# Kernel tuning notes

Hardware: AMD Instinct MI355X
Metric: run time of the kernel (lower is better)

Reference implementation:

```python
import jax, jax.numpy as jnp
import numpy as np

B, LT, LE, D, H, M, BS = 4, 2048, 1024, 1024, 16, 4096, 128
HD = D // H            # head dim 64
NB = LT // BS          # 16 blocks
SINK_ITERS = 5
NEG = -1e9
SCALE = 1.0 / np.sqrt(HD).astype(np.float32)


def setup_inputs() -> dict:
    key = jax.random.key(0)
    ks = jax.random.split(key, 16)
    p = lambda k, shp: jax.random.normal(k, shp, jnp.float32) * 0.02
    return {
        "targets": jax.random.normal(ks[0], (B, LT, D), jnp.float32),
        "encoded": jax.random.normal(ks[1], (B, LE, D), jnp.float32),
        "ln1_s": jnp.ones((D,), jnp.float32), "ln1_b": jnp.zeros((D,), jnp.float32),
        "ln2_s": jnp.ones((D,), jnp.float32), "ln2_b": jnp.zeros((D,), jnp.float32),
        "ln3_s": jnp.ones((D,), jnp.float32), "ln3_b": jnp.zeros((D,), jnp.float32),
        "wq1": p(ks[2], (D, H, HD)), "wk1": p(ks[3], (D, H, HD)),
        "wv1": p(ks[4], (D, H, HD)), "wo1": p(ks[5], (H, HD, D)),
        "wsort": p(ks[6], (H, HD, NB)),
        "wq2": p(ks[7], (D, H, HD)), "wk2": p(ks[8], (D, H, HD)),
        "wv2": p(ks[9], (D, H, HD)), "wo2": p(ks[10], (H, HD, D)),
        "w1": p(ks[11], (D, M)), "b1": jnp.zeros((M,), jnp.float32),
        "w2": p(ks[12], (M, D)), "b2": jnp.zeros((D,), jnp.float32),
    }


def layer_norm(x, s, b, eps=1e-6):
    mu = jnp.mean(x, -1, keepdims=True)
    var = jnp.mean(jnp.square(x - mu), -1, keepdims=True)
    return (x - mu) * jax.lax.rsqrt(var + eps) * s + b


def causal_sinkhorn(logits):
    # logits: [B,H,NB,NB]. Causal block mask + iterative log-space row/col
    # normalization -> soft (doubly-stochastic-ish) block permutation matrix.
    mask = jnp.tril(jnp.ones((NB, NB), bool))
    la = jnp.where(mask, logits, NEG)
    for _ in range(SINK_ITERS):
        la = la - jax.nn.logsumexp(la, axis=-1, keepdims=True)
        la = jnp.where(mask, la, NEG)
        la = la - jax.nn.logsumexp(la, axis=-2, keepdims=True)
        la = jnp.where(mask, la, NEG)
    return jnp.exp(la)


def sinkhorn_self_attention(x, wq, wk, wv, wsort, wo):
    # x: [B,LT,D] -> blocked q/k/v: [B,NB,BS,H,HD]
    q = jnp.einsum('bld,dhk->blhk', x, wq).reshape(B, NB, BS, H, HD)
    k = jnp.einsum('bld,dhk->blhk', x, wk).reshape(B, NB, BS, H, HD)
    v = jnp.einsum('bld,dhk->blhk', x, wv).reshape(B, NB, BS, H, HD)
    # SortNet: sum-pooled block key representations -> block-to-block logits
    krep = jnp.sum(k, axis=2)                                   # [B,NB,H,HD]
    P = causal_sinkhorn(jnp.einsum('bnhk,hkm->bhnm', krep, wsort))  # [B,H,NB,NB]
    ks = jnp.einsum('bhij,bjshk->bishk', P, k)                  # sorted key blocks
    vs = jnp.einsum('bhij,bjshk->bishk', P, v)
    # each query block attends to (own block [causal]) ++ (sorted block)
    s_loc = jnp.einsum('bnqhk,bnshk->bhnqs', q, k) * SCALE      # [B,H,NB,BS,BS]
    s_srt = jnp.einsum('bnqhk,bnshk->bhnqs', q, ks) * SCALE
    cm = jnp.tril(jnp.ones((BS, BS), bool))
    s_loc = jnp.where(cm, s_loc, NEG)
    w = jax.nn.softmax(jnp.concatenate([s_loc, s_srt], axis=-1), axis=-1)
    o = (jnp.einsum('bhnqs,bnshk->bnqhk', w[..., :BS], v)
         + jnp.einsum('bhnqs,bnshk->bnqhk', w[..., BS:], vs))
    return jnp.einsum('blhk,hkd->bld', o.reshape(B, LT, H, HD), wo)


def cross_attention(x, kv, wq, wk, wv, wo):
    q = jnp.einsum('bld,dhk->blhk', x, wq)
    k = jnp.einsum('bld,dhk->blhk', kv, wk)
    v = jnp.einsum('bld,dhk->blhk', kv, wv)
    w = jax.nn.softmax(jnp.einsum('bqhk,bshk->bhqs', q, k) * SCALE, axis=-1)
    o = jnp.einsum('bhqs,bshk->bqhk', w, v)
    return jnp.einsum('blhk,hkd->bld', o, wo)


def reference(targets, encoded, ln1_s, ln1_b, ln2_s, ln2_b, ln3_s, ln3_b,
              wq1, wk1, wv1, wo1, wsort, wq2, wk2, wv2, wo2, w1, b1, w2, b2):
    x = layer_norm(targets, ln1_s, ln1_b)
    x = sinkhorn_self_attention(x, wq1, wk1, wv1, wsort, wo1) + targets
    y = layer_norm(x, ln2_s, ln2_b)
    y = cross_attention(y, encoded, wq2, wk2, wv2, wo2) + x
    z = layer_norm(y, ln3_s, ln3_b)
    z = jnp.dot(jax.nn.gelu(jnp.dot(z, w1) + b1), w2) + b2
    return y + z
```

## Files before the change

### kernel.cpp

```cpp
#include <hip/hip_runtime.h>

typedef unsigned short u16;
typedef unsigned int u32;
typedef __attribute__((ext_vector_type(8))) short short8;
typedef __attribute__((ext_vector_type(4))) short short4_t;
typedef __attribute__((ext_vector_type(4))) float float4_t;

#define B_ 4
#define LT_ 2048
#define LE_ 1024
#define D_ 1024
#define H_ 16
#define HD_ 64
#define NB_ 16
#define BS_ 128
#define M_ 4096
#define SCALE_ 0.125f

typedef __attribute__((address_space(1))) const void gas_t;
typedef __attribute__((address_space(3))) void las_t;

__device__ __forceinline__ float b2f(u16 u) {
  union { unsigned int i; float f; } v; v.i = ((unsigned int)u) << 16; return v.f;
}
__device__ __forceinline__ u16 f2b(float f) {
  union { float f; unsigned int i; } v; v.f = f;
  unsigned int x = v.i;
  return (u16)((x + 0x7fffu + ((x >> 16) & 1u)) >> 16);
}
__device__ __forceinline__ float gelu_f(float u) {
  float t = 0.7978845608028654f * (u + 0.044715f * u * u * u);
  float th = 1.f - 2.f / (__expf(2.f * t) + 1.f);
  return 0.5f * u * (1.f + th);
}
__device__ __forceinline__ void store_val(u16* p, float x) { *p = f2b(x); }
__device__ __forceinline__ void store_val(float* p, float x) { *p = x; }

__global__ __launch_bounds__(256)
void conv_k(const float* __restrict__ in, u16* __restrict__ out) {
  int i = (blockIdx.x * 256 + threadIdx.x) * 4;
  float4_t v = *(const float4_t*)(in + i);
  short4_t o;
  o[0] = (short)f2b(v[0]); o[1] = (short)f2b(v[1]);
  o[2] = (short)f2b(v[2]); o[3] = (short)f2b(v[3]);
  *(short4_t*)(out + i) = o;
}

__global__ __launch_bounds__(256)
void transpose_k(const float* __restrict__ in, u16* __restrict__ out, int R, int rstride) {
  __shared__ u16 tile[32][33];
  int bx = blockIdx.x * 32, by = blockIdx.y * 32;
  int tx = threadIdx.x & 31, ty = threadIdx.x >> 5;
  #pragma unroll
  for (int y = ty; y < 32; y += 8)
    tile[y][tx] = f2b(in[(size_t)(by + y) * rstride + bx + tx]);
  __syncthreads();
  #pragma unroll
  for (int y = ty; y < 32; y += 8)
    out[(size_t)(bx + y) * R + by + tx] = tile[tx][y];
}

#define NJOBS 10
struct TJobs {
  const float* src[NJOBS];
  u16* dst[NJOBS];
  int outR[NJOBS];
  int inS[NJOBS];
  int ntx[NJOBS];
  int ntiles[NJOBS];
};

__global__ __launch_bounds__(256)
void prep_k(TJobs J) {
  int t = blockIdx.x, j = 0;
  while (t >= J.ntiles[j]) { t -= J.ntiles[j]; ++j; }
  const float* in = J.src[j];
  u16* out = J.dst[j];
  const int R = J.outR[j], rstride = J.inS[j];
  const int bx = (t % J.ntx[j]) * 32, by = (t / J.ntx[j]) * 32;
  __shared__ u16 tile[32][33];
  int tx = threadIdx.x & 31, ty = threadIdx.x >> 5;
  #pragma unroll
  for (int y = ty; y < 32; y += 8)
    tile[y][tx] = f2b(in[(size_t)(by + y) * rstride + bx + tx]);
  __syncthreads();
  #pragma unroll
  for (int y = ty; y < 32; y += 8)
    out[(size_t)(bx + y) * R + by + tx] = tile[tx][y];
}

__global__ __launch_bounds__(256)
void ln_k(const float* __restrict__ x, const float* __restrict__ sw,
          const float* __restrict__ bw, u16* __restrict__ out) {
  int row = blockIdx.x, tid = threadIdx.x;
  const float* xr = x + (size_t)row * 1024 + tid * 4;
  float4_t raw = *(const float4_t*)xr;
  float v0 = raw[0], v1 = raw[1], v2 = raw[2], v3 = raw[3];
  float sum = v0 + v1 + v2 + v3;
  #pragma unroll
  for (int off = 32; off > 0; off >>= 1) sum += __shfl_down(sum, off, 64);
  __shared__ float sA[4], sB[4];
  int w = tid >> 6;
  if ((tid & 63) == 0) sA[w] = sum;
  __syncthreads();
  float mu = (sA[0] + sA[1] + sA[2] + sA[3]) * (1.f / 1024.f);
  float d0 = v0 - mu, d1 = v1 - mu, d2 = v2 - mu, d3 = v3 - mu;
  float s2 = d0 * d0 + d1 * d1 + d2 * d2 + d3 * d3;
  #pragma unroll
  for (int off = 32; off > 0; off >>= 1) s2 += __shfl_down(s2, off, 64);
  if ((tid & 63) == 0) sB[w] = s2;
  __syncthreads();
  float inv = rsqrtf((sB[0] + sB[1] + sB[2] + sB[3]) * (1.f / 1024.f) + 1e-6f);
  float4_t sv = *(const float4_t*)(sw + tid * 4);
  float4_t bv = *(const float4_t*)(bw + tid * 4);
  short4_t ov;
  ov[0] = (short)f2b(d0 * inv * sv[0] + bv[0]);
  ov[1] = (short)f2b(d1 * inv * sv[1] + bv[1]);
  ov[2] = (short)f2b(d2 * inv * sv[2] + bv[2]);
  ov[3] = (short)f2b(d3 * inv * sv[3] + bv[3]);
  *(short4_t*)(out + (size_t)row * 1024 + tid * 4) = ov;
}

template<int EPI, typename TC, int SPLIT>
__global__ __launch_bounds__(256)
void gemm_k(const u16* __restrict__ A, const u16* __restrict__ Bt,
            const float* __restrict__ bias, const float* __restrict__ res,
            TC* __restrict__ C, int M, int N, int K, size_t cstride) {
  __shared__ __align__(16) u16 lA[128 * 32];
  __shared__ __align__(16) u16 lB[128 * 32];
  const int gx = gridDim.x;
  int lin = blockIdx.y * gx + blockIdx.x;
  const int nwg = gx * gridDim.y;
  if (!(nwg & 7)) {
    const int chunk = nwg >> 3;
    lin = (lin & 7) * chunk + (lin >> 3);
  }
  const int bn = (lin % gx) * 128;
  const int bm = (lin / gx) * 128;
  const int tid = threadIdx.x;
  const int lane = tid & 63;
  const int wave = tid >> 6;
  const int wy = wave >> 1, wx = wave & 1;
  const int quad = lane >> 4, l16 = lane & 15;

  float4_t acc[4][4];
  float4_t zz = {0.f, 0.f, 0.f, 0.f};
  #pragma unroll
  for (int i = 0; i < 4; ++i)
    #pragma unroll
    for (int j = 0; j < 4; ++j) acc[i][j] = zz;

  const int r0 = tid >> 2, kc0 = (tid & 3) * 8;
  const u16* gA0 = A + (size_t)(bm + r0) * K + kc0;
  const u16* gA1 = A + (size_t)(bm + 64 + r0) * K + kc0;
  const u16* gB0 = Bt + (size_t)(bn + r0) * K + kc0;
  const u16* gB1 = Bt + (size_t)(bn + 64 + r0) * K + kc0;
  u16* lA0 = &lA[tid * 8];
  u16* lA1 = &lA[(tid + 256) * 8];
  u16* lB0 = &lB[tid * 8];
  u16* lB1 = &lB[(tid + 256) * 8];

  for (int k0 = 0; k0 < K; k0 += 32) {
    __syncthreads();
    __builtin_amdgcn_global_load_lds((gas_t*)(gA0 + k0), (las_t*)lA0, 16, 0, 0);
    __builtin_amdgcn_global_load_lds((gas_t*)(gA1 + k0), (las_t*)lA1, 16, 0, 0);
    __builtin_amdgcn_global_load_lds((gas_t*)(gB0 + k0), (las_t*)lB0, 16, 0, 0);
    __builtin_amdgcn_global_load_lds((gas_t*)(gB1 + k0), (las_t*)lB1, 16, 0, 0);
    __syncthreads();
    short8 af[4], bfr[4];
    #pragma unroll
    for (int i = 0; i < 4; ++i)
      af[i] = *(const short8*)&lA[(wy * 64 + i * 16 + l16) * 32 + quad * 8];
    #pragma unroll
    for (int j = 0; j < 4; ++j)
      bfr[j] = *(const short8*)&lB[(wx * 64 + j * 16 + l16) * 32 + quad * 8];
    #pragma unroll
    for (int i = 0; i < 4; ++i)
      #pragma unroll
      for (int j = 0; j < 4; ++j)
        acc[i][j] = __builtin_amdgcn_mfma_f32_16x16x32_bf16(af[i], bfr[j], acc[i][j], 0, 0, 0);
  }

  #pragma unroll
  for (int i = 0; i < 4; ++i) {
    int row = bm + wy * 64 + i * 16 + quad * 4;
    #pragma unroll
    for (int j = 0; j < 4; ++j) {
      int col = bn + wx * 64 + j * 16 + l16;
      TC* Cb = SPLIT ? (C + (size_t)(col >> 10) * cstride) : C;
      int ccol = SPLIT ? (col & 1023) : col;
      int cn = SPLIT ? 1024 : N;
      #pragma unroll
      for (int v = 0; v < 4; ++v) {
        float x = acc[i][j][v];
        size_t idx = (size_t)(row + v) * cn + ccol;
        if (EPI == 1) {
          x += res[idx];
        } else if (EPI == 2) {
          x = gelu_f(x + bias[col]);
        } else if (EPI == 3) {
          x += bias[col] + res[idx];
        }
        store_val(&Cb[idx], x);
      }
    }
  }
}

template<int EPI, typename TC, int SPLIT>
__global__ __launch_bounds__(512, 2)
void gemm256_k(const u16* __restrict__ A, const u16* __restrict__ Bt,
               const float* __restrict__ bias, const float* __restrict__ res,
               TC* __restrict__ C, int M, int N, int K, size_t cstride) {
  __shared__ __align__(16) u16 lA[4][256 * 32];
  __shared__ __align__(16) u16 lB[4][256 * 32];
  const int gx = gridDim.x;
  int lin = blockIdx.y * gx + blockIdx.x;
  const int nwg = gx * gridDim.y;
  if (!(nwg & 7)) {
    const int chunk = nwg >> 3;
    lin = (lin & 7) * chunk + (lin >> 3);
  }
  const int bn = (lin % gx) * 256;
  const int bm = (lin / gx) * 256;
  const int tid = threadIdx.x;
  const int lane = tid & 63;
  const int wave = tid >> 6;
  const int wy = wave >> 2, wx = wave & 3;
  const int quad = lane >> 4, l16 = lane & 15;
  const int slo = ((quad ^ ((l16 >> 1) & 3)) << 4);

  int lrow[2], kcs[2];
  #pragma unroll
  for (int u = 0; u < 2; ++u) {
    int p = (tid + u * 512) * 16;
    int lg = p ^ (((p >> 7) & 3) << 4);
    lrow[u] = lg >> 6;
    kcs[u] = (lg & 63) >> 1;
  }
  const u16* gA[2]; const u16* gB[2];
  #pragma unroll
  for (int u = 0; u < 2; ++u) {
    gA[u] = A + (size_t)(bm + lrow[u]) * K + kcs[u];
    gB[u] = Bt + (size_t)(bn + lrow[u]) * K + kcs[u];
  }
  const int NT = K >> 5;

  float4_t acc[8][4];
  float4_t zz = {0.f, 0.f, 0.f, 0.f};
  #pragma unroll
  for (int i = 0; i < 8; ++i)
    #pragma unroll
    for (int j = 0; j < 4; ++j) acc[i][j] = zz;

  #define STAGE256(TT, BUF)                                                      \
    {                                                                            \
      int kk_ = (TT) * 32;                                                       \
      __builtin_amdgcn_global_load_lds((gas_t*)(gA[0] + kk_),                    \
          (las_t*)((char*)&lA[BUF][0] + tid * 16), 16, 0, 0);                    \
      __builtin_amdgcn_global_load_lds((gas_t*)(gA[1] + kk_),                    \
          (las_t*)((char*)&lA[BUF][0] + (tid + 512) * 16), 16, 0, 0);            \
      __builtin_amdgcn_global_load_lds((gas_t*)(gB[0] + kk_),                    \
          (las_t*)((char*)&lB[BUF][0] + tid * 16), 16, 0, 0);                    \
      __builtin_amdgcn_global_load_lds((gas_t*)(gB[1] + kk_),                    \
          (las_t*)((char*)&lB[BUF][0] + (tid + 512) * 16), 16, 0, 0);            \
    }

  STAGE256(0, 0)
  STAGE256(1, 1)
  STAGE256(2, 2)

  for (int t = 0; t < NT; ++t) {
    asm volatile("s_waitcnt vmcnt(8)" ::: "memory");
    __builtin_amdgcn_s_barrier();
    __builtin_amdgcn_sched_barrier(0);
    int ts = t + 3; if (ts > NT - 1) ts = NT - 1;
    STAGE256(ts, (t + 3) & 3)
    const char* bufA = (const char*)&lA[t & 3][0];
    const char* bufB = (const char*)&lB[t & 3][0];
    short8 af[8], bf[4];
    #pragma unroll
    for (int i = 0; i < 8; ++i)
      af[i] = *(const short8*)(bufA + (wy * 128 + i * 16 + l16) * 64 + slo);
    #pragma unroll
    for (int j = 0; j < 4; ++j)
      bf[j] = *(const short8*)(bufB + (wx * 64 + j * 16 + l16) * 64 + slo);
    __builtin_amdgcn_s_setprio(1);
    #pragma unroll
    for (int i = 0; i < 8; ++i)
      #pragma unroll
      for (int j = 0; j < 4; ++j)
        acc[i][j] = __builtin_amdgcn_mfma_f32_16x16x32_bf16(af[i], bf[j], acc[i][j], 0, 0, 0);
    __builtin_amdgcn_s_setprio(0);
  }
  #undef STAGE256

  #pragma unroll
  for (int i = 0; i < 8; ++i) {
    int row = bm + wy * 128 + i * 16 + quad * 4;
    #pragma unroll
    for (int j = 0; j < 4; ++j) {
      int col = bn + wx * 64 + j * 16 + l16;
      TC* Cb = SPLIT ? (C + (size_t)(col >> 10) * cstride) : C;
      int ccol = SPLIT ? (col & 1023) : col;
      int cn = SPLIT ? 1024 : N;
      #pragma unroll
      for (int v = 0; v < 4; ++v) {
        float x = acc[i][j][v];
        size_t idx = (size_t)(row + v) * cn + ccol;
        if (EPI == 1) {
          x += res[idx];
        } else if (EPI == 2) {
          x = gelu_f(x + bias[col]);
        } else if (EPI == 3) {
          x += bias[col] + res[idx];
        }
        store_val(&Cb[idx], x);
      }
    }
  }
}

__global__ __launch_bounds__(256)
void krep_k(const u16* __restrict__ K1, float* __restrict__ krep) {
  int idx = blockIdx.x * 256 + threadIdx.x;
  int col = idx & 1023;
  int bn = idx >> 10;
  const u16* p = K1 + (size_t)bn * 128 * 1024 + col;
  float s = 0.f;
  for (int i = 0; i < 128; ++i) s += b2f(p[(size_t)i * 1024]);
  krep[idx] = s;
}

__global__ __launch_bounds__(256)
void sinkhorn_k(const float* __restrict__ krep, const float* __restrict__ wsort,
                float* __restrict__ P) {
  int bh = blockIdx.x;
  int b = bh >> 4, h = bh & 15;
  int t = threadIdx.x;
  int i = t >> 4, j = t & 15;
  __shared__ float la[16][17];
  __shared__ float red[16];
  float acc = 0.f;
  const float* kr = krep + ((size_t)b * 16 + i) * 1024 + h * 64;
  const float* ws = wsort + (size_t)h * 64 * 16 + j;
  for (int k = 0; k < 64; ++k) acc += kr[k] * ws[k * 16];
  la[i][j] = (j <= i) ? acc : -1e9f;
  __syncthreads();
  for (int it = 0; it < 5; ++it) {
    if (t < 16) {
      float m = -1e30f;
      for (int jj = 0; jj < 16; ++jj) m = fmaxf(m, la[t][jj]);
      float s = 0.f;
      for (int jj = 0; jj < 16; ++jj) s += __expf(la[t][jj] - m);
      red[t] = m + __logf(s);
    }
    __syncthreads();
    la[i][j] = (j <= i) ? la[i][j] - red[i] : -1e9f;
    __syncthreads();
    if (t < 16) {
      float m = -1e30f;
      for (int ii = 0; ii < 16; ++ii) m = fmaxf(m, la[ii][t]);
      float s = 0.f;
      for (int ii = 0; ii < 16; ++ii) s += __expf(la[ii][t] - m);
      red[t] = m + __logf(s);
    }
    __syncthreads();
    la[i][j] = (j <= i) ? la[i][j] - red[j] : -1e9f;
    __syncthreads();
  }
  P[((size_t)bh * 16 + i) * 16 + j] = __expf(la[i][j]);
}

__global__ __launch_bounds__(256)
void sortmix_k(const float* __restrict__ P, const u16* __restrict__ K1,
               const u16* __restrict__ V1, u16* __restrict__ KS,
               u16* __restrict__ VS) {
  int t = blockIdx.x * 256 + threadIdx.x;
  int col = (t & 127) * 8;
  int rest = t >> 7;
  int b = rest >> 11, is = rest & 2047, i = is >> 7, s = is & 127;
  int h = col >> 6;
  const float* Pr = P + (((size_t)(b * 16 + h)) * 16 + i) * 16;
  size_t base = ((size_t)(b * 2048 + s)) * 1024 + col;
  float ka[8] = {0, 0, 0, 0, 0, 0, 0, 0}, va[8] = {0, 0, 0, 0, 0, 0, 0, 0};
  for (int j = 0; j <= i; ++j) {
    float p = Pr[j];
    short8 kk = *(const short8*)&K1[base + (size_t)j * 131072];
    short8 vv = *(const short8*)&V1[base + (size_t)j * 131072];
    #pragma unroll
    for (int e = 0; e < 8; ++e) {
      ka[e] += p * b2f((u16)kk[e]);
      va[e] += p * b2f((u16)vv[e]);
    }
  }
  size_t ob = ((size_t)(b * 2048 + i * 128 + s)) * 1024 + col;
  short8 ok, ov;
  #pragma unroll
  for (int e = 0; e < 8; ++e) { ok[e] = (short)f2b(ka[e]); ov[e] = (short)f2b(va[e]); }
  *(short8*)&KS[ob] = ok;
  *(short8*)&VS[ob] = ov;
}

template<int CROSS>
__global__ __launch_bounds__(256)
void attn_mfma_k(const u16* __restrict__ Q, const u16* __restrict__ Ka,
                 const u16* __restrict__ Va, const u16* __restrict__ Kb2,
                 const u16* __restrict__ Vb2, u16* __restrict__ O) {
  __shared__ __align__(16) u16 kls[128 * 64];
  __shared__ __align__(16) u16 vlin[128 * 64];
  __shared__ __align__(16) u16 vtls[64 * 128];
  int blk = blockIdx.x;
  {
    int nwg = gridDim.x;
    if (!(nwg & 7)) { int ch = nwg >> 3; blk = (blk & 7) * ch + (blk >> 3); }
  }
  const int n = blk & 15, h = (blk >> 4) & 15, b = blk >> 8;
  const int tid = threadIdx.x, lane = tid & 63, wv = tid >> 6;
  const int quad = lane >> 4, l16 = lane & 15;
  const int m0 = wv * 32;
  const size_t qrowbase = (size_t)b * 2048 + n * 128;

  short8 qa[2][2];
  #pragma unroll
  for (int qi = 0; qi < 2; ++qi)
    #pragma unroll
    for (int ks = 0; ks < 2; ++ks)
      qa[qi][ks] = *(const short8*)&Q[(qrowbase + m0 + qi * 16 + l16) * 1024 +
                                      h * 64 + ks * 32 + quad * 8];

  float4_t acc_o[2][4];
  float mrow[2], lrow[2];
  #pragma unroll
  for (int mi = 0; mi < 2; ++mi) {
    #pragma unroll
    for (int dn = 0; dn < 4; ++dn) acc_o[mi][dn] = {0.f, 0.f, 0.f, 0.f};
    mrow[mi] = -1e30f; lrow[mi] = 0.f;
  }

  const int NT = CROSS ? 8 : 2;
  for (int t = 0; t < NT; ++t) {
    const u16 *Kg, *Vg;
    bool causal = false;
    if (CROSS) {
      size_t kb = ((size_t)b * 1024 + t * 128) * 1024 + h * 64;
      Kg = Ka + kb; Vg = Va + kb;
    } else if (t == 0) {
      size_t kb = qrowbase * 1024 + h * 64;
      Kg = Ka + kb; Vg = Va + kb; causal = true;
    } else {
      size_t kb = qrowbase * 1024 + h * 64;
      Kg = Kb2 + kb; Vg = Vb2 + kb;
    }
    #pragma unroll
    for (int i = 0; i < 4; ++i) {
      int c = tid + i * 256;
      int row = c >> 3, slot = c & 7, dd = slot * 8;
      short8 kv8 = *(const short8*)&Kg[(size_t)row * 1024 + dd];
      *(short8*)&kls[row * 64 + ((slot ^ (row & 7)) * 8)] = kv8;
      short8 vv8 = *(const short8*)&Vg[(size_t)row * 1024 + dd];
      *(short8*)&vlin[row * 64 + dd] = vv8;
    }
    __syncthreads();

    #pragma unroll
    for (int ii = 0; ii < 4; ++ii) {
      int d = tid & 63;
      int kvg = (tid >> 6) * 4 + ii;
      union { short8 s8; u16 us[8]; } tt;
      #pragma unroll
      for (int j = 0; j < 8; ++j)
        tt.us[j] = vlin[(kvg * 8 + j) * 64 + d];
      int slotp = (kvg & 8) | ((kvg ^ (d & 7)) & 7);
      *(short8*)&vtls[d * 128 + slotp * 8] = tt.s8;
    }

    float4_t s[2][8];
    #pragma unroll
    for (int qi = 0; qi < 2; ++qi)
      #pragma unroll
      for (int nj = 0; nj < 8; ++nj) s[qi][nj] = {0.f, 0.f, 0.f, 0.f};
    #pragma unroll
    for (int nj = 0; nj < 8; ++nj) {
      int r = nj * 16 + l16;
      short8 k0 = *(const short8*)&kls[r * 64 + ((quad ^ (l16 & 7)) * 8)];
      short8 k1 = *(const short8*)&kls[r * 64 + (((4 + quad) ^ (l16 & 7)) * 8)];
      #pragma unroll
      for (int qi = 0; qi < 2; ++qi) {
        s[qi][nj] = __builtin_amdgcn_mfma_f32_16x16x32_bf16(k0, qa[qi][0], s[qi][nj], 0, 0, 0);
        s[qi][nj] = __builtin_amdgcn_mfma_f32_16x16x32_bf16(k1, qa[qi][1], s[qi][nj], 0, 0, 0);
      }
    }

    float crv[2];
    u32 p01[2][8], p23[2][8];
    #pragma unroll
    for (int qi = 0; qi < 2; ++qi) {
      const int qrow = m0 + qi * 16 + l16;
      float mx = -1e30f;
      #pragma unroll
      for (int nj = 0; nj < 8; ++nj)
        #pragma unroll
        for (int v = 0; v < 4; ++v) {
          float x = s[qi][nj][v] * SCALE_;
          if (causal && (nj * 16 + quad * 4 + v > qrow)) x = -1e30f;
          s[qi][nj][v] = x;
          mx = fmaxf(mx, x);
        }
      mx = fmaxf(mx, __shfl_xor(mx, 16, 64));
      mx = fmaxf(mx, __shfl_xor(mx, 32, 64));
      float mn = fmaxf(mrow[qi], mx);
      crv[qi] = __expf(mrow[qi] - mn);
      mrow[qi] = mn;
      float rs = 0.f;
      #pragma unroll
      for (int nj = 0; nj < 8; ++nj)
        #pragma unroll
        for (int v = 0; v < 4; ++v) {
          float p = __expf(s[qi][nj][v] - mn);
          s[qi][nj][v] = p;
          rs += p;
        }
      rs += __shfl_xor(rs, 16, 64);
      rs += __shfl_xor(rs, 32, 64);
      lrow[qi] = lrow[qi] * crv[qi] + rs;
      #pragma unroll
      for (int nj = 0; nj < 8; ++nj) {
        p01[qi][nj] = (u32)f2b(s[qi][nj][0]) | ((u32)f2b(s[qi][nj][1]) << 16);
        p23[qi][nj] = (u32)f2b(s[qi][nj][2]) | ((u32)f2b(s[qi][nj][3]) << 16);
      }
    }
    #pragma unroll
    for (int mi = 0; mi < 2; ++mi)
      #pragma unroll
      for (int v = 0; v < 4; ++v) {
        float c = __shfl(crv[mi], quad * 20 + v, 64);
        #pragma unroll
        for (int dn = 0; dn < 4; ++dn) acc_o[mi][dn][v] *= c;
      }

    __syncthreads();

    const int src0 = (quad & 1) * 32 + l16;
    const int src1 = src0 + 16;
    const bool hi = (quad >> 1) != 0;
    #pragma unroll
    for (int ks = 0; ks < 4; ++ks) {
      union { short8 s8; u32 u[4]; } au[2];
      #pragma unroll
      for (int qi = 0; qi < 2; ++qi) {
        u32 w0a = __shfl(p01[qi][2 * ks],     src0, 64);
        u32 w0b = __shfl(p01[qi][2 * ks + 1], src0, 64);
        u32 w1a = __shfl(p23[qi][2 * ks],     src0, 64);
        u32 w1b = __shfl(p23[qi][2 * ks + 1], src0, 64);
        u32 w2a = __shfl(p01[qi][2 * ks],     src1, 64);
        u32 w2b = __shfl(p01[qi][2 * ks + 1], src1, 64);
        u32 w3a = __shfl(p23[qi][2 * ks],     src1, 64);
        u32 w3b = __shfl(p23[qi][2 * ks + 1], src1, 64);
        au[qi].u[0] = hi ? w0b : w0a;
        au[qi].u[1] = hi ? w1b : w1a;
        au[qi].u[2] = hi ? w2b : w2a;
        au[qi].u[3] = hi ? w3b : w3a;
      }
      #pragma unroll
      for (int dn = 0; dn < 4; ++dn) {
        int dR = dn * 16 + l16;
        int sbase = ks * 4 + quad;
        int sp = (sbase & 8) | ((sbase ^ (l16 & 7)) & 7);
        short8 bv = *(const short8*)&vtls[dR * 128 + sp * 8];
        acc_o[0][dn] = __builtin_amdgcn_mfma_f32_16x16x32_bf16(au[0].s8, bv, acc_o[0][dn], 0, 0, 0);
        acc_o[1][dn] = __builtin_amdgcn_mfma_f32_16x16x32_bf16(au[1].s8, bv, acc_o[1][dn], 0, 0, 0);
      }
    }
  }
  #pragma unroll
  for (int mi = 0; mi < 2; ++mi) {
    float invl = 1.f / lrow[mi];
    #pragma unroll
    for (int v = 0; v < 4; ++v) {
      float inv = __shfl(invl, quad * 20 + v, 64);
      int rowl = m0 + mi * 16 + quad * 4 + v;
      #pragma unroll
      for (int dn = 0; dn < 4; ++dn)
        O[(qrowbase + rowl) * 1024 + h * 64 + dn * 16 + l16] =
            f2b(acc_o[mi][dn][v] * inv);
    }
  }
}

extern "C" void kernel_launch(void* const* d_in, const int* in_sizes, int n_in,
                              void* d_out, int out_size, void* d_ws, size_t ws_size,
                              hipStream_t stream) {
  const float* targets = (const float*)d_in[0];
  const float* encoded = (const float*)d_in[1];
  const float* ln1s = (const float*)d_in[2];
  const float* ln1b = (const float*)d_in[3];
  const float* ln2s = (const float*)d_in[4];
  const float* ln2b = (const float*)d_in[5];
  const float* ln3s = (const float*)d_in[6];
  const float* ln3b = (const float*)d_in[7];
  const float* wq1 = (const float*)d_in[8];
  const float* wk1 = (const float*)d_in[9];
  const float* wv1 = (const float*)d_in[10];
  const float* wo1 = (const float*)d_in[11];
  const float* wsort = (const float*)d_in[12];
  const float* wq2 = (const float*)d_in[13];
  const float* wk2 = (const float*)d_in[14];
  const float* wv2 = (const float*)d_in[15];
  const float* wo2 = (const float*)d_in[16];
  const float* w1 = (const float*)d_in[17];
  const float* b1 = (const float*)d_in[18];
  const float* w2 = (const float*)d_in[19];
  const float* b2 = (const float*)d_in[20];
  float* out = (float*)d_out;
  (void)in_sizes; (void)n_in; (void)out_size;

  char* ws = (char*)d_ws;
  size_t off = 0;
  auto alloc = [&](size_t n) -> char* {
    char* p = ws + off;
    off += (n + 255) & ~(size_t)255;
    return p;
  };

  const size_t NTD = (size_t)B_ * LT_ * D_;
  const size_t NEED_BIG = (size_t)(8 * 2 + 8 + 8) * 1024 * 1024
                        + (size_t)LE_ * B_ * D_ * 2
                        + NTD * 2 * 7
                        + (1u << 20);

  if (ws_size >= NEED_BIG) {
    u16* wq1t = (u16*)alloc((size_t)1024 * 1024 * 2);
    u16* wk1t = (u16*)alloc((size_t)1024 * 1024 * 2);
    u16* wv1t = (u16*)alloc((size_t)1024 * 1024 * 2);
    u16* wo1t = (u16*)alloc((size_t)1024 * 1024 * 2);
    u16* wq2t = (u16*)alloc((size_t)1024 * 1024 * 2);
    u16* wk2t = (u16*)alloc((size_t)1024 * 1024 * 2);
    u16* wv2t = (u16*)alloc((size_t)1024 * 1024 * 2);
    u16* wo2t = (u16*)alloc((size_t)1024 * 1024 * 2);
    u16* w1t = (u16*)alloc((size_t)4096 * 1024 * 2);
    u16* w2t = (u16*)alloc((size_t)1024 * 4096 * 2);
    u16* Eb  = (u16*)alloc((size_t)B_ * LE_ * D_ * 2);
    u16* XLN = (u16*)alloc(NTD * 2);
    u16* Qb  = (u16*)alloc(NTD * 2);
    u16* Kb  = (u16*)alloc(NTD * 2);
    u16* Vb  = (u16*)alloc(NTD * 2);
    u16* KSb = (u16*)alloc(NTD * 2);
    u16* VSb = (u16*)alloc(NTD * 2);
    u16* Ob  = (u16*)alloc(NTD * 2);
    float* KREP = (float*)alloc((size_t)B_ * NB_ * 1024 * 4);
    float* Pm = (float*)alloc((size_t)B_ * H_ * NB_ * NB_ * 4);
    u16* HML = Qb;

    TJobs J;
    const float* srcs[NJOBS] = {wq1, wk1, wv1, wo1, wq2, wk2, wv2, wo2, w1, w2};
    u16* dsts[NJOBS] = {wq1t, wk1t, wv1t, wo1t, wq2t, wk2t, wv2t, wo2t, w1t, w2t};
    int total = 0;
    for (int j = 0; j < NJOBS; ++j) {
      J.src[j] = srcs[j]; J.dst[j] = dsts[j];
      if (j < 8)      { J.outR[j] = 1024; J.inS[j] = 1024; J.ntx[j] = 32;  J.ntiles[j] = 1024; }
      else if (j == 8){ J.outR[j] = 1024; J.inS[j] = 4096; J.ntx[j] = 128; J.ntiles[j] = 4096; }
      else            { J.outR[j] = 4096; J.inS[j] = 1024; J.ntx[j] = 32;  J.ntiles[j] = 4096; }
      total += J.ntiles[j];
    }
    prep_k<<<total, 256, 0, stream>>>(J);
    conv_k<<<4096, 256, 0, stream>>>(encoded, Eb);

    ln_k<<<8192, 256, 0, stream>>>(targets, ln1s, ln1b, XLN);
    gemm256_k<0, u16, 1><<<dim3(12, 32), 512, 0, stream>>>(XLN, wq1t, nullptr, nullptr,
                                                           Qb, 8192, 3072, 1024, NTD);
    krep_k<<<256, 256, 0, stream>>>(Kb, KREP);
    sinkhorn_k<<<64, 256, 0, stream>>>(KREP, wsort, Pm);
    sortmix_k<<<4096, 256, 0, stream>>>(Pm, Kb, Vb, KSb, VSb);
    attn_mfma_k<0><<<1024, 256, 0, stream>>>(Qb, Kb, Vb, KSb, VSb, Ob);
    gemm_k<1, float, 0><<<dim3(8, 64), 256, 0, stream>>>(Ob, wo1t, nullptr, targets, out, 8192, 1024, 1024, 0);
    ln_k<<<8192, 256, 0, stream>>>(out, ln2s, ln2b, XLN);
    gemm_k<0, u16, 0><<<dim3(8, 64), 256, 0, stream>>>(XLN, wq2t, nullptr, nullptr, Qb, 8192, 1024, 1024, 0);
    gemm_k<0, u16, 1><<<dim3(16, 32), 256, 0, stream>>>(Eb, wk2t, nullptr, nullptr, Kb, 4096, 2048, 1024, NTD);
    attn_mfma_k<1><<<1024, 256, 0, stream>>>(Qb, Kb, Vb, nullptr, nullptr, Ob);
    gemm_k<1, float, 0><<<dim3(8, 64), 256, 0, stream>>>(Ob, wo2t, nullptr, out, out, 8192, 1024, 1024, 0);
    ln_k<<<8192, 256, 0, stream>>>(out, ln3s, ln3b, XLN);
    gemm256_k<2, u16, 0><<<dim3(16, 32), 512, 0, stream>>>(XLN, w1t, b1, nullptr, HML, 8192, 4096, 1024, 0);
    gemm_k<3, float, 0><<<dim3(8, 64), 256, 0, stream>>>(HML, w2t, b2, out, out, 8192, 1024, 4096, 0);
    return;
  }

  const size_t SLC = (size_t)LT_ * D_;
  u16* wT  = (u16*)alloc((size_t)1024 * 1024 * 2);
  u16* XLN = (u16*)alloc(SLC * 2);
  u16* Qb  = (u16*)alloc(SLC * 2);
  u16* Kb  = (u16*)alloc(SLC * 2);
  u16* Vb  = (u16*)alloc(SLC * 2);
  u16* KSb = (u16*)alloc(SLC * 2);
  u16* VSb = (u16*)alloc(SLC * 2);
  u16* Ob  = (u16*)alloc(SLC * 2);
  u16* Hc  = (u16*)alloc(SLC * 2);
  u16* Eb  = (u16*)alloc((size_t)LE_ * D_ * 2);
  float* KREP = (float*)alloc((size_t)NB_ * 1024 * 4);
  float* Pm = (float*)alloc((size_t)H_ * NB_ * NB_ * 4);

  auto T = [&](const float* src, int rs) {
    transpose_k<<<dim3(32, 32), 256, 0, stream>>>(src, wT, 1024, rs);
  };

  for (int b = 0; b < B_; ++b) {
    const float* tgt_b = targets + (size_t)b * SLC;
    const float* enc_b = encoded + (size_t)b * LE_ * D_;
    float* out_b = out + (size_t)b * SLC;

    ln_k<<<2048, 256, 0, stream>>>(tgt_b, ln1s, ln1b, XLN);
    T(wq1, 1024);
    gemm_k<0, u16, 0><<<dim3(8, 16), 256, 0, stream>>>(XLN, wT, nullptr, nullptr, Qb, 2048, 1024, 1024, 0);
    T(wk1, 1024);
    gemm_k<0, u16, 0><<<dim3(8, 16), 256, 0, stream>>>(XLN, wT, nullptr, nullptr, Kb, 2048, 1024, 1024, 0);
    T(wv1, 1024);
    gemm_k<0, u16, 0><<<dim3(8, 16), 256, 0, stream>>>(XLN, wT, nullptr, nullptr, Vb, 2048, 1024, 1024, 0);
    krep_k<<<64, 256, 0, stream>>>(Kb, KREP);
    sinkhorn_k<<<16, 256, 0, stream>>>(KREP, wsort, Pm);
    sortmix_k<<<1024, 256, 0, stream>>>(Pm, Kb, Vb, KSb, VSb);
    attn_mfma_k<0><<<256, 256, 0, stream>>>(Qb, Kb, Vb, KSb, VSb, Ob);
    T(wo1, 1024);
    gemm_k<1, float, 0><<<dim3(8, 16), 256, 0, stream>>>(Ob, wT, nullptr, tgt_b, out_b, 2048, 1024, 1024, 0);
    ln_k<<<2048, 256, 0, stream>>>(out_b, ln2s, ln2b, XLN);
    conv_k<<<1024, 256, 0, stream>>>(enc_b, Eb);
    T(wq2, 1024);
    gemm_k<0, u16, 0><<<dim3(8, 16), 256, 0, stream>>>(XLN, wT, nullptr, nullptr, Qb, 2048, 1024, 1024, 0);
    T(wk2, 1024);
    gemm_k<0, u16, 0><<<dim3(8, 8), 256, 0, stream>>>(Eb, wT, nullptr, nullptr, Kb, 1024, 1024, 1024, 0);
    T(wv2, 1024);
    gemm_k<0, u16, 0><<<dim3(8, 8), 256, 0, stream>>>(Eb, wT, nullptr, nullptr, Vb, 1024, 1024, 1024, 0);
    attn_mfma_k<1><<<256, 256, 0, stream>>>(Qb, Kb, Vb, nullptr, nullptr, Ob);
    T(wo2, 1024);
    gemm_k<1, float, 0><<<dim3(8, 16), 256, 0, stream>>>(Ob, wT, nullptr, out_b, out_b, 2048, 1024, 1024, 0);
    ln_k<<<2048, 256, 0, stream>>>(out_b, ln3s, ln3b, XLN);
    for (int c = 0; c < 4; ++c) {
      T(w1 + (size_t)c * 1024, 4096);
      gemm_k<2, u16, 0><<<dim3(8, 16), 256, 0, stream>>>(XLN, wT, b1 + c * 1024, nullptr, Hc,
                                                         2048, 1024, 1024, 0);
      T(w2 + (size_t)c * 1024 * 1024, 1024);
      if (c < 3)
        gemm_k<1, float, 0><<<dim3(8, 16), 256, 0, stream>>>(Hc, wT, nullptr, out_b, out_b,
                                                             2048, 1024, 1024, 0);
      else
        gemm_k<3, float, 0><<<dim3(8, 16), 256, 0, stream>>>(Hc, wT, b2, out_b, out_b,
                                                             2048, 1024, 1024, 0);
    }
  }
}
```

Baseline: 860.5 us.

## Add 4-stage pipelined 128x128 GEMM kernel and use it for five projections

Adds a new 128x128-tile GEMM kernel that keeps four LDS buffers and issues global-to-LDS loads three K-steps ahead. It waits on vmcnt instead of a full sync and raises wave priority around the MFMA block. It also remaps workgroup IDs in chunks of eight for locality. It replaces the single-buffered gemm_k in the output projections, cross-attention Q/KV projections and FFN down projection, aiming to hide global load latency. In exchange it uses more LDS (64KB per block), which may reduce occupancy, and relies on hand-tuned waitcnt correctness.

New measurement: 777.2 us. 1.11x faster.

```diff
diff --git a/kernel.cpp b/kernel.cpp
--- a/kernel.cpp
+++ b/kernel.cpp
@@ -180,6 +180,110 @@
       for (int j = 0; j < 4; ++j)
         acc[i][j] = __builtin_amdgcn_mfma_f32_16x16x32_bf16(af[i], bfr[j], acc[i][j], 0, 0, 0);
   }
+
+  #pragma unroll
+  for (int i = 0; i < 4; ++i) {
+    int row = bm + wy * 64 + i * 16 + quad * 4;
+    #pragma unroll
+    for (int j = 0; j < 4; ++j) {
+      int col = bn + wx * 64 + j * 16 + l16;
+      TC* Cb = SPLIT ? (C + (size_t)(col >> 10) * cstride) : C;
+      int ccol = SPLIT ? (col & 1023) : col;
+      int cn = SPLIT ? 1024 : N;
+      #pragma unroll
+      for (int v = 0; v < 4; ++v) {
+        float x = acc[i][j][v];
+        size_t idx = (size_t)(row + v) * cn + ccol;
+        if (EPI == 1) {
+          x += res[idx];
+        } else if (EPI == 2) {
+          x = gelu_f(x + bias[col]);
+        } else if (EPI == 3) {
+          x += bias[col] + res[idx];
+        }
+        store_val(&Cb[idx], x);
+      }
+    }
+  }
+}
+
+template<int EPI, typename TC, int SPLIT>
+__global__ __launch_bounds__(256, 2)
+void gemm128d_k(const u16* __restrict__ A, const u16* __restrict__ Bt,
+                const float* __restrict__ bias, const float* __restrict__ res,
+                TC* __restrict__ C, int M, int N, int K, size_t cstride) {
+  __shared__ __align__(16) u16 lA[4][128 * 32];
+  __shared__ __align__(16) u16 lB[4][128 * 32];
+  const int gx = gridDim.x;
+  int lin = blockIdx.y * gx + blockIdx.x;
+  const int nwg = gx * gridDim.y;
+  if (!(nwg & 7)) {
+    const int chunk = nwg >> 3;
+    lin = (lin & 7) * chunk + (lin >> 3);
+  }
+  const int bn = (lin % gx) * 128;
+  const int bm = (lin / gx) * 128;
+  const int tid = threadIdx.x;
+  const int lane = tid & 63;
+  const int wave = tid >> 6;
+  const int wy = wave >> 1, wx = wave & 1;
+  const int quad = lane >> 4, l16 = lane & 15;
+
+  float4_t acc[4][4];
+  float4_t zz = {0.f, 0.f, 0.f, 0.f};
+  #pragma unroll
+  for (int i = 0; i < 4; ++i)
+    #pragma unroll
+    for (int j = 0; j < 4; ++j) acc[i][j] = zz;
+
+  const int r0 = tid >> 2, kc0 = (tid & 3) * 8;
+  const u16* gA0 = A + (size_t)(bm + r0) * K + kc0;
+  const u16* gA1 = A + (size_t)(bm + 64 + r0) * K + kc0;
+  const u16* gB0 = Bt + (size_t)(bn + r0) * K + kc0;
+  const u16* gB1 = Bt + (size_t)(bn + 64 + r0) * K + kc0;
+  const int NT = K >> 5;
+
+  #define STAGE128(TT, BUF)                                                      \
+    {                                                                            \
+      int kk_ = (TT) * 32;                                                       \
+      __builtin_amdgcn_global_load_lds((gas_t*)(gA0 + kk_),                      \
+          (las_t*)&lA[BUF][tid * 8], 16, 0, 0);                                  \
+      __builtin_amdgcn_global_load_lds((gas_t*)(gA1 + kk_),                      \
+          (las_t*)&lA[BUF][(tid + 256) * 8], 16, 0, 0);                          \
+      __builtin_amdgcn_global_load_lds((gas_t*)(gB0 + kk_),                      \
+          (las_t*)&lB[BUF][tid * 8], 16, 0, 0);                                  \
+      __builtin_amdgcn_global_load_lds((gas_t*)(gB1 + kk_),                      \
+          (las_t*)&lB[BUF][(tid + 256) * 8], 16, 0, 0);                          \
+    }
+
+  STAGE128(0, 0)
+  STAGE128(1, 1)
+  STAGE128(2, 2)
+
+  for (int t = 0; t < NT; ++t) {
+    asm volatile("s_waitcnt vmcnt(8)" ::: "memory");
+    __builtin_amdgcn_s_barrier();
+    __builtin_amdgcn_sched_barrier(0);
+    int ts = t + 3; if (ts > NT - 1) ts = NT - 1;
+    STAGE128(ts, (t + 3) & 3)
+    const u16* bufA = &lA[t & 3][0];
+    const u16* bufB = &lB[t & 3][0];
+    short8 af[4], bfr[4];
+    #pragma unroll
+    for (int i = 0; i < 4; ++i)
+      af[i] = *(const short8*)&bufA[(wy * 64 + i * 16 + l16) * 32 + quad * 8];
+    #pragma unroll
+    for (int j = 0; j < 4; ++j)
+      bfr[j] = *(const short8*)&bufB[(wx * 64 + j * 16 + l16) * 32 + quad * 8];
+    __builtin_amdgcn_s_setprio(1);
+    #pragma unroll
+    for (int i = 0; i < 4; ++i)
+      #pragma unroll
+      for (int j = 0; j < 4; ++j)
+        acc[i][j] = __builtin_amdgcn_mfma_f32_16x16x32_bf16(af[i], bfr[j], acc[i][j], 0, 0, 0);
+    __builtin_amdgcn_s_setprio(0);
+  }
+  #undef STAGE128
 
   #pragma unroll
   for (int i = 0; i < 4; ++i) {
@@ -673,15 +777,15 @@
     sinkhorn_k<<<64, 256, 0, stream>>>(KREP, wsort, Pm);
     sortmix_k<<<4096, 256, 0, stream>>>(Pm, Kb, Vb, KSb, VSb);
     attn_mfma_k<0><<<1024, 256, 0, stream>>>(Qb, Kb, Vb, KSb, VSb, Ob);
-    gemm_k<1, float, 0><<<dim3(8, 64), 256, 0, stream>>>(Ob, wo1t, nullptr, targets, out, 8192, 1024, 1024, 0);
+    gemm128d_k<1, float, 0><<<dim3(8, 64), 256, 0, stream>>>(Ob, wo1t, nullptr, targets, out, 8192, 1024, 1024, 0);
     ln_k<<<8192, 256, 0, stream>>>(out, ln2s, ln2b, XLN);
-    gemm_k<0, u16, 0><<<dim3(8, 64), 256, 0, stream>>>(XLN, wq2t, nullptr, nullptr, Qb, 8192, 1024, 1024, 0);
-    gemm_k<0, u16, 1><<<dim3(16, 32), 256, 0, stream>>>(Eb, wk2t, nullptr, nullptr, Kb, 4096, 2048, 1024, NTD);
+    gemm128d_k<0, u16, 0><<<dim3(8, 64), 256, 0, stream>>>(XLN, wq2t, nullptr, nullptr, Qb, 8192, 1024, 1024, 0);
+    gemm128d_k<0, u16, 1><<<dim3(16, 32), 256, 0, stream>>>(Eb, wk2t, nullptr, nullptr, Kb, 4096, 2048, 1024, NTD);
     attn_mfma_k<1><<<1024, 256, 0, stream>>>(Qb, Kb, Vb, nullptr, nullptr, Ob);
-    gemm_k<1, float, 0><<<dim3(8, 64), 256, 0, stream>>>(Ob, wo2t, nullptr, out, out, 8192, 1024, 1024, 0);
+    gemm128d_k<1, float, 0><<<dim3(8, 64), 256, 0, stream>>>(Ob, wo2t, nullptr, out, out, 8192, 1024, 1024, 0);
     ln_k<<<8192, 256, 0, stream>>>(out, ln3s, ln3b, XLN);
     gemm256_k<2, u16, 0><<<dim3(16, 32), 512, 0, stream>>>(XLN, w1t, b1, nullptr, HML, 8192, 4096, 1024, 0);
-    gemm_k<3, float, 0><<<dim3(8, 64), 256, 0, stream>>>(HML, w2t, b2, out, out, 8192, 1024, 4096, 0);
+    gemm128d_k<3, float, 0><<<dim3(8, 64), 256, 0, stream>>>(HML, w2t, b2, out, out, 8192, 1024, 4096, 0);
     return;
   }
 
```
